# Kernel tuning notes

Hardware: AMD Instinct MI355X
Metric: run time of the kernel (lower is better)

## Reference

```python
import jax, jax.numpy as jnp
import numpy as np
import math

B, H, S, DK = 4, 16, 2048, 64

def setup_inputs() -> dict:
    key = jax.random.key(0)
    kq, kk, kv, km = jax.random.split(key, 4)
    q = jax.random.normal(kq, (B, H, S, DK), dtype=jnp.float32)
    k = jax.random.normal(kk, (B, H, S, DK), dtype=jnp.float32)
    v = jax.random.normal(kv, (B, H, S, DK), dtype=jnp.float32)
    mask = jax.random.randint(km, (B, 1, 1, S), 0, 2, dtype=jnp.int32)
    return {"q": q, "k": k, "v": v, "mask": mask}

def reference(q, k, v, mask):
    scale = 1.0 / math.sqrt(DK)
    # scores: [B, H, S, S]
    scores = jnp.einsum('bhqd,bhkd->bhqk', q, k) * scale
    scores = jnp.where(mask == 0, jnp.float32(-1e9), scores)
    attn = jax.nn.softmax(scores, axis=-1)
    out = jnp.einsum('bhqk,bhkd->bhqd', attn, v)
    return out
```

## Files before the change

### kernel.cpp

```cpp
#include <hip/hip_runtime.h>
#include <hip/hip_bf16.h>

#define S_LEN 2048
#define D_K   64
#define N_H   16
#define N_B   4
#define KVT   32
#define NBH   (N_B * N_H)
#define WS_NEED (2L * NBH * S_LEN * D_K * 2 + 4L * S_LEN * 4 + 16)

typedef __attribute__((ext_vector_type(8)))  short bf16x8;
typedef __attribute__((ext_vector_type(16))) float f32x16;
typedef unsigned int u32;
typedef __attribute__((ext_vector_type(4))) u32 u32x4;

__device__ inline short f2bfs(float x) {
    __hip_bfloat16 h = __float2bfloat16(x);
    return __builtin_bit_cast(short, h);
}

__device__ inline bf16x8 cvt8(const float* __restrict__ p) {
    float4 a = *(const float4*)p;
    float4 b = *(const float4*)(p + 4);
    bf16x8 f;
    f[0] = f2bfs(a.x); f[1] = f2bfs(a.y);
    f[2] = f2bfs(a.z); f[3] = f2bfs(a.w);
    f[4] = f2bfs(b.x); f[5] = f2bfs(b.y);
    f[6] = f2bfs(b.z); f[7] = f2bfs(b.w);
    return f;
}

__device__ inline bf16x8 cvt8s(const float* __restrict__ p, float s) {
    float4 a = *(const float4*)p;
    float4 b = *(const float4*)(p + 4);
    bf16x8 f;
    f[0] = f2bfs(a.x * s); f[1] = f2bfs(a.y * s);
    f[2] = f2bfs(a.z * s); f[3] = f2bfs(a.w * s);
    f[4] = f2bfs(b.x * s); f[5] = f2bfs(b.y * s);
    f[6] = f2bfs(b.z * s); f[7] = f2bfs(b.w * s);
    return f;
}

__device__ inline int vswz(int d) { return ((d & 7) ^ ((d >> 3) & 7)) << 4; }

__device__ inline void gld16(const void* g, void* l) {
    __builtin_amdgcn_global_load_lds(
        (const __attribute__((address_space(1))) void*)g,
        (__attribute__((address_space(3))) void*)l, 16, 0, 0);
}

__global__ __launch_bounds__(256)
void gather_cvt(const float* __restrict__ k, const float* __restrict__ v,
                const int* __restrict__ mask, const int dummy,
                short* __restrict__ kc, short* __restrict__ vt,
                int* __restrict__ cnt) {
    const int bid = blockIdx.x, bh = bid >> 5, i0 = (bid & 31) * 64;
    const int b = bh >> 4;
    const int t = threadIdx.x;

    __shared__ __align__(16) short tile_[64][72];
    __shared__ int idx_s[64];
    __shared__ int m_s;

    if (t < 64) {
        const int lane = t;
        const int* mb = mask + b * S_LEN;
        int base = 0;
#pragma unroll 4
        for (int j0 = 0; j0 < S_LEN; j0 += 64) {
            int mv = mb[j0 + lane];
            unsigned long long ball = __ballot(mv != 0);
            int pos = base + __popcll(ball & ((1ull << lane) - 1ull));
            if (mv && pos >= i0 && pos < i0 + 64) idx_s[pos - i0] = j0 + lane;
            base += __popcll(ball);
        }
        if (lane == 0) m_s = base;
    }
    __syncthreads();
    const int m = m_s;
    if (t == 0 && i0 == 0) cnt[b] = m;
    if (i0 >= ((m + 63) & ~63)) return;

    const int r = t >> 2, c0 = (t & 3) * 16;
    const int i = i0 + r;

    bf16x8 fv0, fv1, fk0, fk1;
    if (i < m) {
        const int src = idx_s[r];
        const float* kp = k + ((long)bh * S_LEN + src) * D_K + c0;
        const float* vp = v + ((long)bh * S_LEN + src) * D_K + c0;
        fk0 = cvt8(kp); fk1 = cvt8(kp + 8);
        fv0 = cvt8(vp); fv1 = cvt8(vp + 8);
    } else {
#pragma unroll
        for (int j = 0; j < 8; ++j) { fk0[j] = 0; fk1[j] = 0; fv0[j] = 0; fv1[j] = 0; }
    }
    short* kdst = kc + ((long)bh * S_LEN + i) * D_K + c0;
    *(bf16x8*)kdst       = fk0;
    *(bf16x8*)(kdst + 8) = fk1;
    *(bf16x8*)&tile_[r][c0]     = fv0;
    *(bf16x8*)&tile_[r][c0 + 8] = fv1;
    __syncthreads();
    const int dd = t >> 2, k0 = (t & 3) * 16;
    bf16x8 h0, h1;
#pragma unroll
    for (int j = 0; j < 8; ++j) {
        h0[j] = tile_[k0 + j][dd];
        h1[j] = tile_[k0 + 8 + j][dd];
    }
    short* dst = vt + ((long)bh * D_K + dd) * S_LEN + i0 + k0;
    *(bf16x8*)dst       = h0;
    *(bf16x8*)(dst + 8) = h1;
}

__global__ __launch_bounds__(256)
void attn_fwd(const float* __restrict__ q, const short* __restrict__ kbf,
              const short* __restrict__ vtb, const int* __restrict__ cnt,
              float* __restrict__ out) {
    const int id      = blockIdx.x;
    const int logical = (id & 7) * 128 + (id >> 3);
    const int bh      = logical >> 4;
    const int qb4     = logical & 15;
    const int b       = bh >> 4;
    const int t       = threadIdx.x;
    const int lane    = t & 63;
    const int wq      = t >> 6;
    const int hb      = lane >> 5;
    const int ql      = lane & 31;

    const int m   = cnt[b];
    const int NTr = (m + KVT - 1) >> 5;

    __shared__ __align__(16) char lds[4][8192];
    char* kl = &lds[wq][0];
    char* vl = &lds[wq][4096];

    const float scale2 = 0.125f * 1.44269504f;
    const long  baseq  = (long)bh * S_LEN * D_K;
    const int   qrow0  = qb4 * 128 + wq * 32;

    bf16x8 qf[4];
    {
        const float* qp = q + baseq + (long)(qrow0 + ql) * D_K + hb * 8;
#pragma unroll
        for (int kd = 0; kd < 4; ++kd) qf[kd] = cvt8s(qp + kd * 16, scale2);
    }

    const int krow_ = lane >> 3, kchk_ = lane & 7;
    const short* ks0 = kbf + baseq + (long)krow_ * D_K
                       + ((kchk_ ^ (krow_ & 7)) * 8);
    const int vd_ = lane >> 2, vc_ = lane & 3;
    const short* vs0 = vtb + ((long)bh * D_K + vd_) * S_LEN
                       + ((vc_ ^ ((vd_ >> 1) & 3)) * 8);

    auto STAGE = [&](int tile) {
        const short* kp = ks0 + (long)tile * (KVT * D_K);
        const short* vp = vs0 + tile * KVT;
#pragma unroll
        for (int i = 0; i < 4; ++i)
            gld16(kp + i * (8 * D_K), kl + i * 1024);
#pragma unroll
        for (int i = 0; i < 4; ++i)
            gld16(vp + (long)i * 16 * S_LEN, vl + i * 1024);
    };

    f32x16 o0, o1;
#pragma unroll
    for (int r = 0; r < 16; ++r) { o0[r] = 0.f; o1[r] = 0.f; }
    float lpart = 0.f;

    f32x16 ZEROV;
#pragma unroll
    for (int r = 0; r < 16; ++r) ZEROV[r] = 0.f;

    STAGE(0);

    for (int tt = 0; tt < NTr; ++tt) {
        asm volatile("s_waitcnt vmcnt(0)" ::: "memory");
        __builtin_amdgcn_sched_barrier(0);

        f32x16 st;
        {
            const int sz = (ql & 7) << 4;
            const int rb = ql * 128;
            bf16x8 kf0 = *(const bf16x8*)(kl + (rb + ((hb * 8) * 2) ^ 0 ? 0 : 0, (rb + (((0 * 16 + hb * 8) * 2)) ^ sz)));
            f32x16 a;
            __builtin_amdgcn_s_setprio(1);
            {
                bf16x8 kf = *(const bf16x8*)(kl + ((rb + (hb * 8) * 2) ^ sz));
                if (tt + 1 < NTr) {
                    a = __builtin_amdgcn_mfma_f32_32x32x16_bf16(kf, qf[0], ZEROV, 0, 0, 0);
                } else {
                    f32x16 c0;
                    int keyb = tt * KVT + 4 * hb;
#pragma unroll
                    for (int r = 0; r < 16; ++r) {
                        int key = keyb + (r & 3) + 8 * (r >> 2);
                        c0[r] = (key < m) ? 0.f : -1e9f;
                    }
                    a = __builtin_amdgcn_mfma_f32_32x32x16_bf16(kf, qf[0], c0, 0, 0, 0);
                }
            }
#pragma unroll
            for (int kd = 1; kd < 4; ++kd) {
                bf16x8 kf = *(const bf16x8*)(kl + ((rb + (kd * 16 + hb * 8) * 2) ^ sz));
                a = __builtin_amdgcn_mfma_f32_32x32x16_bf16(kf, qf[kd], a, 0, 0, 0);
            }
            __builtin_amdgcn_s_setprio(0);
            st = a;
        }

        u32 w[8];
        {
            float rs0 = 0.f, rs1 = 0.f;
#pragma unroll
            for (int mm = 0; mm < 8; ++mm) {
                float p0 = __builtin_amdgcn_exp2f(st[2 * mm]);
                float p1 = __builtin_amdgcn_exp2f(st[2 * mm + 1]);
                rs0 += p0; rs1 += p1;
                u32 r;
                asm("v_cvt_pk_bf16_f32 %0, %1, %2" : "=v"(r) : "v"(p0), "v"(p1));
                w[mm] = r;
            }
            lpart += rs0 + rs1;
        }

#pragma unroll
        for (int kbi = 0; kbi < 2; ++kbi) {
            int a2 = kbi * 4;
            u32 x0 = w[a2 + 0], y0 = w[a2 + 2];
            u32 x1 = w[a2 + 1], y1 = w[a2 + 3];
            asm("v_permlane32_swap_b32 %0, %1" : "+v"(x0), "+v"(y0));
            asm("v_permlane32_swap_b32 %0, %1" : "+v"(x1), "+v"(y1));
            u32x4 av = {x0, x1, y0, y1};
            bf16x8 pa = __builtin_bit_cast(bf16x8, av);
            __builtin_amdgcn_s_setprio(1);
#pragma unroll
            for (int dn = 0; dn < 2; ++dn) {
                int d = dn * 32 + ql;
                int byte = d * 64 + (((kbi * 16 + hb * 8) * 2) ^ (((ql >> 1) & 3) << 4));
                bf16x8 vf = *(const bf16x8*)(vl + byte);
                if (dn == 0)
                    o0 = __builtin_amdgcn_mfma_f32_32x32x16_bf16(pa, vf, o0, 0, 0, 0);
                else
                    o1 = __builtin_amdgcn_mfma_f32_32x32x16_bf16(pa, vf, o1, 0, 0, 0);
            }
            __builtin_amdgcn_s_setprio(0);
        }

        if (tt + 1 < NTr) {
            asm volatile("s_waitcnt lgkmcnt(0)" ::: "memory");
            __builtin_amdgcn_sched_barrier(0);
            STAGE(tt + 1);
        }
    }

    float lrun = lpart + __shfl_xor(lpart, 32, 64);
    float rl = 1.0f / lrun;
#pragma unroll
    for (int r = 0; r < 16; ++r) {
        int   cr  = (r & 3) + 8 * (r >> 2) + 4 * hb;
        float rlr = __shfl(rl, cr, 64);
        long  rowb = baseq + (long)(qrow0 + cr) * D_K;
        out[rowb + ql]      = o0[r] * rlr;
        out[rowb + 32 + ql] = o1[r] * rlr;
    }
}

__global__ __launch_bounds__(256)
void attn_fwd_legacy(const float* __restrict__ q, const float* __restrict__ k,
                     const float* __restrict__ v, const int* __restrict__ mask,
                     float* __restrict__ out) {
    const int id      = blockIdx.x;
    const int logical = (id & 7) * 128 + (id >> 3);
    const int bh      = logical >> 4;
    const int qblk    = logical & 15;
    const int b       = bh >> 4;
    const int t       = threadIdx.x;
    const int lane    = t & 63;
    const int wq      = t >> 6;
    const int hb      = lane >> 5;
    const int ql      = lane & 31;

    __shared__ __align__(16) short kbuf[64 * D_K];
    __shared__ __align__(16) short vtbuf[D_K * 64];
    __shared__ float mbias[S_LEN];

    const float scale2 = 0.125f * 1.44269504f;
    const long  base   = (long)bh * S_LEN * D_K;
    const int   qrow0  = qblk * 128 + wq * 32;

    {
        const int* mb = mask + b * S_LEN;
        for (int i = t; i < S_LEN; i += 256)
            mbias[i] = mb[i] ? 0.f : -1.442695e9f;
    }

    bf16x8 qf[4];
    {
        const float* qp = q + base + (long)(qrow0 + ql) * D_K + hb * 8;
#pragma unroll
        for (int kd = 0; kd < 4; ++kd) qf[kd] = cvt8s(qp + kd * 16, 1.0f);
    }

    f32x16 o0, o1;
#pragma unroll
    for (int r = 0; r < 16; ++r) { o0[r] = 0.f; o1[r] = 0.f; }
    float mrun = -1e30f, lrun = 0.f;

    const int srow = t >> 3;
    const int scol = t & 7;
    float4 kr[2][2], vr[2][2];

    auto LOADT = [&](int kv0) {
#pragma unroll
        for (int u2 = 0; u2 < 2; ++u2) {
            int row = srow + u2 * 32;
            const float* kp = k + base + (long)(kv0 + row) * D_K + scol * 8;
            const float* vp = v + base + (long)(kv0 + row) * D_K + scol * 8;
            kr[u2][0] = *(const float4*)kp; kr[u2][1] = *(const float4*)(kp + 4);
            vr[u2][0] = *(const float4*)vp; vr[u2][1] = *(const float4*)(vp + 4);
        }
    };

    LOADT(0);

    for (int tt = 0; tt < S_LEN / 64; ++tt) {
        const int kv0 = tt * 64;
        __syncthreads();
#pragma unroll
        for (int u2 = 0; u2 < 2; ++u2) {
            int row = srow + u2 * 32;
            bf16x8 fk, fv;
#pragma unroll
            for (int j = 0; j < 4; ++j) {
                fk[j]     = f2bfs(((const float*)&kr[u2][0])[j]);
                fk[j + 4] = f2bfs(((const float*)&kr[u2][1])[j]);
                fv[j]     = f2bfs(((const float*)&vr[u2][0])[j]);
                fv[j + 4] = f2bfs(((const float*)&vr[u2][1])[j]);
            }
            int kbyte = (row * 128 + scol * 16) ^ ((row & 7) << 4);
            *(bf16x8*)((char*)kbuf + kbyte) = fk;
#pragma unroll
            for (int j = 0; j < 8; ++j) {
                int d = scol * 8 + j;
                *(short*)((char*)vtbuf + ((d * 128 + row * 2) ^ vswz(d))) = fv[j];
            }
        }
        if (tt + 1 < S_LEN / 64) LOADT(kv0 + 64);
        __syncthreads();

        f32x16 stl[2];
#pragma unroll
        for (int kb32 = 0; kb32 < 2; ++kb32) {
            f32x16 acc;
#pragma unroll
            for (int r = 0; r < 16; ++r) acc[r] = 0.f;
            int krow = kb32 * 32 + ql;
            int rb = krow * 128, sz = (krow & 7) << 4;
#pragma unroll
            for (int kd = 0; kd < 4; ++kd) {
                bf16x8 kf = *(const bf16x8*)((const char*)kbuf + ((rb + (kd * 16 + hb * 8) * 2) ^ sz));
                acc = __builtin_amdgcn_mfma_f32_32x32x16_bf16(kf, qf[kd], acc, 0, 0, 0);
            }
            stl[kb32] = acc;
        }
#pragma unroll
        for (int kb32 = 0; kb32 < 2; ++kb32)
#pragma unroll
            for (int r = 0; r < 16; ++r) {
                int key = kv0 + kb32 * 32 + (r & 3) + 8 * (r >> 2) + 4 * hb;
                stl[kb32][r] = fmaf(stl[kb32][r], scale2, mbias[key]);
            }

        float m8[8];
#pragma unroll
        for (int i = 0; i < 8; ++i)
            m8[i] = fmaxf(fmaxf(stl[0][i], stl[0][i + 8]),
                          fmaxf(stl[1][i], stl[1][i + 8]));
        float tmax = fmaxf(fmaxf(fmaxf(m8[0], m8[1]), fmaxf(m8[2], m8[3])),
                           fmaxf(fmaxf(m8[4], m8[5]), fmaxf(m8[6], m8[7])));
        tmax = fmaxf(tmax, __shfl_xor(tmax, 32, 64));

        if (__any(tmax > mrun + 10.0f)) {
            float mnew = fmaxf(mrun, tmax);
            float al   = __builtin_amdgcn_exp2f(mrun - mnew);
            mrun = mnew;
            lrun *= al;
#pragma unroll
            for (int r = 0; r < 16; ++r) {
                float ar = __shfl(al, (r & 3) + 8 * (r >> 2) + 4 * hb, 64);
                o0[r] *= ar; o1[r] *= ar;
            }
        }

        u32 w[2][8];
        float rs = 0.f;
#pragma unroll
        for (int kb32 = 0; kb32 < 2; ++kb32)
#pragma unroll
            for (int mm = 0; mm < 8; ++mm) {
                float p0 = __builtin_amdgcn_exp2f(stl[kb32][2 * mm]     - mrun);
                float p1 = __builtin_amdgcn_exp2f(stl[kb32][2 * mm + 1] - mrun);
                rs += p0 + p1;
                w[kb32][mm] = (u32)(unsigned short)f2bfs(p0) |
                              ((u32)(unsigned short)f2bfs(p1) << 16);
            }
        rs += __shfl_xor(rs, 32, 64);
        lrun += rs;

#pragma unroll
        for (int kbi = 0; kbi < 4; ++kbi) {
            int c = kbi >> 1, a2 = (kbi & 1) * 4;
            u32 x0 = w[c][a2 + 0], y0 = w[c][a2 + 2];
            u32 x1 = w[c][a2 + 1], y1 = w[c][a2 + 3];
            asm("v_permlane32_swap_b32 %0, %1" : "+v"(x0), "+v"(y0));
            asm("v_permlane32_swap_b32 %0, %1" : "+v"(x1), "+v"(y1));
            u32x4 av = {x0, x1, y0, y1};
            bf16x8 pa = __builtin_bit_cast(bf16x8, av);
#pragma unroll
            for (int dn = 0; dn < 2; ++dn) {
                int d = dn * 32 + ql;
                bf16x8 vf = *(const bf16x8*)((const char*)vtbuf +
                              ((d * 128 + (kbi * 16 + hb * 8) * 2) ^ vswz(d)));
                if (dn == 0)
                    o0 = __builtin_amdgcn_mfma_f32_32x32x16_bf16(pa, vf, o0, 0, 0, 0);
                else
                    o1 = __builtin_amdgcn_mfma_f32_32x32x16_bf16(pa, vf, o1, 0, 0, 0);
            }
        }
    }

    float rl = 1.0f / lrun;
#pragma unroll
    for (int r = 0; r < 16; ++r) {
        int   cr  = (r & 3) + 8 * (r >> 2) + 4 * hb;
        float rlr = __shfl(rl, cr, 64);
        long  rowb = base + (long)(qrow0 + cr) * D_K;
        out[rowb + ql]      = o0[r] * rlr;
        out[rowb + 32 + ql] = o1[r] * rlr;
    }
}

extern "C" void kernel_launch(void* const* d_in, const int* in_sizes, int n_in,
                              void* d_out, int out_size, void* d_ws, size_t ws_size,
                              hipStream_t stream) {
    const float* q    = (const float*)d_in[0];
    const float* k    = (const float*)d_in[1];
    const float* v    = (const float*)d_in[2];
    const int*   mask = (const int*)d_in[3];
    float*       out  = (float*)d_out;

    if (ws_size >= (size_t)WS_NEED) {
        short* kc  = (short*)d_ws;
        short* vt  = kc + (long)NBH * S_LEN * D_K;
        int*   cnt = (int*)(vt + (long)NBH * S_LEN * D_K);
        gather_cvt<<<dim3(NBH * (S_LEN / 64)), 256, 0, stream>>>(k, v, mask, 0, kc, vt, cnt);
        attn_fwd<<<dim3((S_LEN / 32) * NBH / 4), 256, 0, stream>>>(q, kc, vt, cnt, out);
    } else {
        attn_fwd_legacy<<<dim3((S_LEN / 128) * NBH), 256, 0, stream>>>(q, k, v, mask, out);
    }
}
```

Before: 87.32 us.

## Stage K/V tiles through registers with one-tile prefetch instead of direct global-to-LDS loads

Replaces the direct global_load_lds staging of K and V tiles with ordinary global loads into registers, issued one tile ahead, followed by explicit LDS writes. The explicit vmcnt/lgkmcnt waits and sched barriers at the top and bottom of the loop are removed, so the next tile's global loads can overlap the current tile's MFMA work. This raises register pressure and adds VGPR-to-LDS store instructions. Synchronisation now relies on the compiler's implicit waits; since each wave seems to read only LDS it wrote itself, correctness depends on that assumption.

New measurement: 92.49 us. 5.9% more time.

```diff
diff --git a/kernel.cpp b/kernel.cpp
--- a/kernel.cpp
+++ b/kernel.cpp
@@ -42,12 +42,6 @@
 }
 
 __device__ inline int vswz(int d) { return ((d & 7) ^ ((d >> 3) & 7)) << 4; }
-
-__device__ inline void gld16(const void* g, void* l) {
-    __builtin_amdgcn_global_load_lds(
-        (const __attribute__((address_space(1))) void*)g,
-        (__attribute__((address_space(3))) void*)l, 16, 0, 0);
-}
 
 __global__ __launch_bounds__(256)
 void gather_cvt(const float* __restrict__ k, const float* __restrict__ v,
@@ -153,15 +147,24 @@
     const short* vs0 = vtb + ((long)bh * D_K + vd_) * S_LEN
                        + ((vc_ ^ ((vd_ >> 1) & 3)) * 8);
 
-    auto STAGE = [&](int tile) {
+    bf16x8 kreg[4], vreg[4];
+    auto LOADR = [&](int tile) {
         const short* kp = ks0 + (long)tile * (KVT * D_K);
         const short* vp = vs0 + tile * KVT;
 #pragma unroll
         for (int i = 0; i < 4; ++i)
-            gld16(kp + i * (8 * D_K), kl + i * 1024);
+            kreg[i] = *(const bf16x8*)(kp + i * (8 * D_K));
 #pragma unroll
         for (int i = 0; i < 4; ++i)
-            gld16(vp + (long)i * 16 * S_LEN, vl + i * 1024);
+            vreg[i] = *(const bf16x8*)(vp + (long)i * 16 * S_LEN);
+    };
+    auto WRITEL = [&]() {
+#pragma unroll
+        for (int i = 0; i < 4; ++i)
+            *(bf16x8*)(kl + i * 1024 + lane * 16) = kreg[i];
+#pragma unroll
+        for (int i = 0; i < 4; ++i)
+            *(bf16x8*)(vl + i * 1024 + lane * 16) = vreg[i];
     };
 
     f32x16 o0, o1;
@@ -173,17 +176,15 @@
 #pragma unroll
     for (int r = 0; r < 16; ++r) ZEROV[r] = 0.f;
 
-    STAGE(0);
+    LOADR(0);
+    WRITEL();
+    if (NTr > 1) LOADR(1);
 
     for (int tt = 0; tt < NTr; ++tt) {
-        asm volatile("s_waitcnt vmcnt(0)" ::: "memory");
-        __builtin_amdgcn_sched_barrier(0);
-
         f32x16 st;
         {
             const int sz = (ql & 7) << 4;
             const int rb = ql * 128;
-            bf16x8 kf0 = *(const bf16x8*)(kl + (rb + ((hb * 8) * 2) ^ 0 ? 0 : 0, (rb + (((0 * 16 + hb * 8) * 2)) ^ sz)));
             f32x16 a;
             __builtin_amdgcn_s_setprio(1);
             {
@@ -249,9 +250,8 @@
         }
 
         if (tt + 1 < NTr) {
-            asm volatile("s_waitcnt lgkmcnt(0)" ::: "memory");
-            __builtin_amdgcn_sched_barrier(0);
-            STAGE(tt + 1);
+            WRITEL();
+            if (tt + 2 < NTr) LOADR(tt + 2);
         }
     }
 
```
